# Optimization experiments

Hardware: AMD Instinct MI355X
Metric: run time of the kernel (lower is better)

## Reference

```python
import jax, jax.numpy as jnp
import numpy as np


def setup_inputs() -> dict:
    key = jax.random.key(0)
    kx, ke = jax.random.split(key)
    N, T, D, M = 64, 400, 1024, 256
    x = jax.random.normal(kx, (N, T, D), dtype=jnp.float32)
    embedding = jax.random.normal(ke, (M, D), dtype=jnp.float32)
    return {"x": x, "embedding": embedding}


def reference(x, embedding):
    # x: (N, T, D); embedding (codebook): (M, D)
    M, D = embedding.shape
    # L2_distance: normalize codebook rows, distances to detached x
    emb_norm = embedding / (jnp.linalg.norm(embedding, axis=1, keepdims=True) + 1e-4)
    x_flat = jax.lax.stop_gradient(x).reshape(-1, D)  # (N*T, D)
    distances = (jnp.sum(emb_norm ** 2, axis=1)[None, :]
                 + jnp.sum(x_flat ** 2, axis=1, keepdims=True)
                 - 2.0 * (x_flat @ emb_norm.T))  # (N*T, M)
    indices = jnp.argmin(distances, axis=-1)  # (N*T,)
    encodings = jax.nn.one_hot(indices, M, dtype=jnp.float32)  # (N*T, M)
    quantized = embedding[indices].reshape(x.shape)  # gather from UNnormalized codebook

    # commitment loss (both sides detached in original -> constant)
    commitment_loss = jnp.mean(
        (jax.lax.stop_gradient(x) - jax.lax.stop_gradient(quantized)) ** 2)

    # straight-through + average with quantized
    quantized_st = x + jax.lax.stop_gradient(quantized - x)
    quantized_ = (quantized_st + quantized) / 2.0

    avg_probs = jnp.mean(encodings, axis=0)  # (M,)
    perplexity = jnp.exp(-jnp.sum(avg_probs * jnp.log(avg_probs + 1e-10)))
    return quantized_, commitment_loss, perplexity
```

## Files before the change

### kernel.cpp

```cpp
#include <hip/hip_runtime.h>
#include <cstdint>
#include <cstddef>


typedef __attribute__((ext_vector_type(8))) short short8;
typedef __attribute__((ext_vector_type(4))) float f32x4;

namespace {
constexpr int kNT = 25600;
constexpr int kD  = 1024;
constexpr int kM  = 256;
constexpr size_t kQElems = (size_t)kNT * kD;

constexpr int WS_IMG_H = 0;
constexpr int WS_IMG_L = 131072;
constexpr int WS_E2N   = 262144;
constexpr int WS_SCL   = WS_E2N + kM;
constexpr int WS_E2R   = WS_SCL + kM;
constexpr int WS_COM   = WS_E2R + kM;
constexpr int WS_HIST  = WS_COM + 4;
constexpr int WS_ZERO_BYTES = (WS_HIST + kM - WS_COM) * 4;
}

typedef __attribute__((address_space(3))) unsigned int        lds_u32;
typedef const __attribute__((address_space(1))) unsigned int  glb_u32;

__device__ __forceinline__ void gl2lds16(const void* g, void* l) {
  __builtin_amdgcn_global_load_lds((glb_u32*)g, (lds_u32*)l, 16, 0, 0);
}

__global__ __launch_bounds__(256) void vq_normalize(const float* __restrict__ emb,
                                                    float* __restrict__ ws) {
  const int m = blockIdx.x;
  const int t = threadIdx.x;
  const float4 v = reinterpret_cast<const float4*>(emb + (size_t)m * kD)[t];
  float s = v.x * v.x + v.y * v.y + v.z * v.z + v.w * v.w;
#pragma unroll
  for (int mask = 32; mask >= 1; mask >>= 1) s += __shfl_xor(s, mask);
  __shared__ float red[4];
  if ((t & 63) == 0) red[t >> 6] = s;
  __syncthreads();
  const float tot = red[0] + red[1] + red[2] + red[3];
  const float sc  = sqrtf(tot) + 1e-4f;
  const float inv = 1.0f / sc;
  const float4 nv = make_float4(v.x * inv, v.y * inv, v.z * inv, v.w * inv);

  float s2 = nv.x * nv.x + nv.y * nv.y + nv.z * nv.z + nv.w * nv.w;
#pragma unroll
  for (int mask = 32; mask >= 1; mask >>= 1) s2 += __shfl_xor(s2, mask);
  __syncthreads();
  if ((t & 63) == 0) red[t >> 6] = s2;
  __syncthreads();
  if (t == 0) {
    ws[WS_E2N + m] = red[0] + red[1] + red[2] + red[3];
    ws[WS_SCL + m] = sc;
    ws[WS_E2R + m] = tot;
  }

  unsigned short* imgh = (unsigned short*)(ws + WS_IMG_H);
  unsigned short* imgl = (unsigned short*)(ws + WS_IMG_L);
  const int c  = t >> 3;
  const int g  = (t >> 1) & 3;
  const int sq = g ^ ((m >> 1) & 3);
  const int base = c * 8192 + m * 32 + sq * 8 + 4 * (t & 1);
  ushort4 hq, lq;
#pragma unroll
  for (int j = 0; j < 4; ++j) {
    const float fv = (&nv.x)[j];
    const unsigned int b = __float_as_uint(fv);
    const unsigned short hi = (unsigned short)(b >> 16);
    const float lof = fv - __uint_as_float(b & 0xFFFF0000u);
    const unsigned short lo = (unsigned short)(__float_as_uint(lof) >> 16);
    (&hq.x)[j] = hi; (&lq.x)[j] = lo;
  }
  *(ushort4*)(imgh + base) = hq;
  *(ushort4*)(imgl + base) = lq;
}

__global__ __launch_bounds__(256, 2) void vq_main(const float* __restrict__ x,
                                                  const float* __restrict__ emb,
                                                  const float* __restrict__ wsc,
                                                  float* __restrict__ out,
                                                  float* __restrict__ commit_sum,
                                                  int* __restrict__ hist) {
  __shared__ char pool[65536];
  __shared__ float e2n_s[kM], scl_s[kM], e2r_s[kM], x2s[64];
  __shared__ int idx_s[64];

  const int t  = threadIdx.x;
  const int l  = t & 63;
  const int w  = t >> 6;
  const int h  = w >> 1;
  const int rw = w & 1;
  const int r0 = blockIdx.x * 64;

  e2n_s[t] = wsc[WS_E2N + t];
  scl_s[t] = wsc[WS_SCL + t];
  e2r_s[t] = wsc[WS_E2R + t];

  const unsigned short* img = (const unsigned short*)(wsc + ((w & 1) ? WS_IMG_L : WS_IMG_H));
  char* myslot = pool + w * 16384;

  const int nlo = l & 15;
  const int sq  = (l >> 4) ^ ((l >> 1) & 3);
  const int rowA   = r0 + rw * 32 + nlo;
  const int kbase0 = h * 512 + ((l >> 4) << 3);

  f32x4 acc[2][16];
#pragma unroll
  for (int rt = 0; rt < 2; ++rt)
#pragma unroll
    for (int ct = 0; ct < 16; ++ct) acc[rt][ct] = (f32x4)0.0f;
  float x2[2] = {0.0f, 0.0f};

#pragma unroll 1
  for (int cc = 0; cc < 16; ++cc) {
    const unsigned short* src = img + (size_t)(h * 16 + cc) * 8192 + l * 8;
#pragma unroll
    for (int it = 0; it < 16; ++it)
      gl2lds16(src + it * 512, myslot + it * 1024);

    float4 f[2][2];
#pragma unroll
    for (int rt = 0; rt < 2; ++rt) {
      const float* xp = x + (size_t)(rowA + rt * 16) * kD + (cc * 32 + kbase0);
      f[rt][0] = *(const float4*)xp;
      f[rt][1] = *(const float4*)(xp + 4);
    }
    __syncthreads();

    short8 ah[2], al[2];
#pragma unroll
    for (int rt = 0; rt < 2; ++rt) {
      union { short8 v; unsigned short u[8]; } H, L;
#pragma unroll
      for (int j = 0; j < 8; ++j) {
        const float fv = (&f[rt][j >> 2].x)[j & 3];
        const unsigned int b = __float_as_uint(fv);
        H.u[j] = (unsigned short)(b >> 16);
        const float lof = fv - __uint_as_float(b & 0xFFFF0000u);
        L.u[j] = (unsigned short)(__float_as_uint(lof) >> 16);
        x2[rt] += fv * fv;
      }
      ah[rt] = H.v; al[rt] = L.v;
    }

    const char* bh_base = pool + (h * 2 + 0) * 16384;
    const char* bl_base = pool + (h * 2 + 1) * 16384;
#pragma unroll
    for (int ct = 0; ct < 16; ++ct) {
      const int off = (ct * 16 + nlo) * 64 + sq * 16;
      const short8 bh = *(const short8*)(bh_base + off);
      const short8 bl = *(const short8*)(bl_base + off);
#pragma unroll
      for (int rt = 0; rt < 2; ++rt) {
        acc[rt][ct] = __builtin_amdgcn_mfma_f32_16x16x32_bf16(ah[rt], bh, acc[rt][ct], 0, 0, 0);
        acc[rt][ct] = __builtin_amdgcn_mfma_f32_16x16x32_bf16(ah[rt], bl, acc[rt][ct], 0, 0, 0);
        acc[rt][ct] = __builtin_amdgcn_mfma_f32_16x16x32_bf16(al[rt], bh, acc[rt][ct], 0, 0, 0);
      }
    }
    __syncthreads();
  }

#pragma unroll
  for (int rt = 0; rt < 2; ++rt) {
    x2[rt] += __shfl_xor(x2[rt], 16);
    x2[rt] += __shfl_xor(x2[rt], 32);
  }

  float* Sd = (float*)pool;
  if (h == 0) {
#pragma unroll
    for (int rt = 0; rt < 2; ++rt) {
#pragma unroll
      for (int ct = 0; ct < 16; ++ct)
#pragma unroll
        for (int rg = 0; rg < 4; ++rg) {
          const int row = rw * 32 + rt * 16 + (l >> 4) * 4 + rg;
          Sd[row * 256 + ct * 16 + nlo] = -2.0f * acc[rt][ct][rg];
        }
      if (l < 16) x2s[rw * 32 + rt * 16 + l] = x2[rt];
    }
  }
  __syncthreads();
  if (h == 1) {
#pragma unroll
    for (int rt = 0; rt < 2; ++rt) {
#pragma unroll
      for (int ct = 0; ct < 16; ++ct)
#pragma unroll
        for (int rg = 0; rg < 4; ++rg) {
          const int row = rw * 32 + rt * 16 + (l >> 4) * 4 + rg;
          Sd[row * 256 + ct * 16 + nlo] -= 2.0f * acc[rt][ct][rg];
        }
      if (l < 16) x2s[rw * 32 + rt * 16 + l] += x2[rt];
    }
  }
  __syncthreads();

  {
    const int row = t >> 2, q = t & 3;
    float bv = 3.0e38f; int bj = 0;
    const float* Sr = Sd + row * 256 + q * 64;
    const float* En = e2n_s + q * 64;
    for (int jj = 0; jj < 64; ++jj) {
      const int jloc = (jj + 2 * row) & 63;
      const float v = En[jloc] + Sr[jloc];
      const int j = q * 64 + jloc;
      if (v < bv || (v == bv && j < bj)) { bv = v; bj = j; }
    }
#pragma unroll
    for (int m = 1; m <= 2; m <<= 1) {
      const float ov = __shfl_xor(bv, m);
      const int   oj = __shfl_xor(bj, m);
      if (ov < bv || (ov == bv && oj < bj)) { bv = ov; bj = oj; }
    }
    if (q == 0) {
      idx_s[row] = bj;
      atomicAdd(&hist[bj], 1);
      const float cl = x2s[row] + e2r_s[bj] - (e2n_s[bj] - bv) * scl_s[bj];
      atomicAdd(commit_sum, cl);
    }
  }
  __syncthreads();

  const float4* emb4 = reinterpret_cast<const float4*>(emb);
  float4* out4 = reinterpret_cast<float4*>(out);
#pragma unroll 4
  for (int i = 0; i < 64; ++i) {
    const int m = idx_s[i];
    out4[(size_t)(r0 + i) * (kD / 4) + t] = emb4[(size_t)m * (kD / 4) + t];
  }
}

__global__ __launch_bounds__(256) void vq_final(const int* __restrict__ hist,
                                                const float* __restrict__ commit_sum,
                                                float* __restrict__ out) {
  const int t = threadIdx.x;
  const float p = (float)hist[t] * (1.0f / (float)kNT);
  float s = p * logf(p + 1e-10f);
#pragma unroll
  for (int mask = 32; mask >= 1; mask >>= 1) s += __shfl_xor(s, mask);
  __shared__ float red[4];
  if ((t & 63) == 0) red[t >> 6] = s;
  __syncthreads();
  if (t == 0) {
    const float ent = red[0] + red[1] + red[2] + red[3];
    out[kQElems]     = commit_sum[0] * (1.0f / (float)kQElems);
    out[kQElems + 1] = expf(-ent);
  }
}

extern "C" void kernel_launch(void* const* d_in, const int* in_sizes, int n_in,
                              void* d_out, int out_size, void* d_ws, size_t ws_size,
                              hipStream_t stream) {
  (void)in_sizes; (void)n_in; (void)out_size; (void)ws_size;
  const float* x   = (const float*)d_in[0];
  const float* emb = (const float*)d_in[1];
  float* out = (float*)d_out;
  float* ws  = (float*)d_ws;

  hipMemsetAsync((char*)d_ws + (size_t)WS_COM * 4, 0, WS_ZERO_BYTES, stream);
  hipLaunchKernelGGL(vq_normalize, dim3(kM), dim3(256), 0, stream, emb, ws);
  hipLaunchKernelGGL(vq_main, dim3(kNT / 64), dim3(256), 0, stream,
                     x, emb, ws, out, ws + WS_COM, (int*)(ws + WS_HIST));
  hipLaunchKernelGGL(vq_final, dim3(1), dim3(256), 0, stream,
                     (const int*)(ws + WS_HIST), ws + WS_COM, out);
}
```

Baseline: 248.2 us.

## Double-buffer codebook tiles and give each wave full K range with register argmin

The main kernel is restructured so each wave owns 16 rows over the full K dimension instead of splitting K across wave pairs. This removes the LDS partial-sum reduction and the shared distance matrix; argmin is done in registers with cross-lane shuffles. Codebook tiles are double-buffered in LDS with async global-to-LDS loads, the next x chunk is prefetched, and hand-placed ds_read/waitcnt/sched_barrier interleave LDS reads with MFMAs. The gather/copy is done per wave. Risks include higher register pressure from 16 accumulators plus 16 prefetched B fragments, and fragile manual waitcnt counts.

```diff
diff --git a/kernel.cpp b/kernel.cpp
--- a/kernel.cpp
+++ b/kernel.cpp
@@ -24,9 +24,17 @@
 
 typedef __attribute__((address_space(3))) unsigned int        lds_u32;
 typedef const __attribute__((address_space(1))) unsigned int  glb_u32;
+typedef const __attribute__((address_space(3))) char          lds_chc;
 
 __device__ __forceinline__ void gl2lds16(const void* g, void* l) {
   __builtin_amdgcn_global_load_lds((glb_u32*)g, (lds_u32*)l, 16, 0, 0);
+}
+
+template <int OFF>
+__device__ __forceinline__ short8 ldsr(lds_chc* p) {
+  short8 r;
+  asm volatile("ds_read_b128 %0, %1 offset:%c2" : "=v"(r) : "v"(p), "i"(OFF));
+  return r;
 }
 
 __global__ __launch_bounds__(256) void vq_normalize(const float* __restrict__ emb,
@@ -77,159 +85,182 @@
   *(ushort4*)(imgl + base) = lq;
 }
 
+
+#define RD8(BSEL, G, H0, H1, H2, H3, L0, L1, L2, L3)                           \
+  H0 = ldsr<(BSEL) * 32768 + ((G) * 4 + 0) * 1024>(lbase);                     \
+  H1 = ldsr<(BSEL) * 32768 + ((G) * 4 + 1) * 1024>(lbase);                     \
+  H2 = ldsr<(BSEL) * 32768 + ((G) * 4 + 2) * 1024>(lbase);                     \
+  H3 = ldsr<(BSEL) * 32768 + ((G) * 4 + 3) * 1024>(lbase);                     \
+  L0 = ldsr<(BSEL) * 32768 + 16384 + ((G) * 4 + 0) * 1024>(lbase);             \
+  L1 = ldsr<(BSEL) * 32768 + 16384 + ((G) * 4 + 1) * 1024>(lbase);             \
+  L2 = ldsr<(BSEL) * 32768 + 16384 + ((G) * 4 + 2) * 1024>(lbase);             \
+  L3 = ldsr<(BSEL) * 32768 + 16384 + ((G) * 4 + 3) * 1024>(lbase);
+
+#define MM12(G, H0, H1, H2, H3, L0, L1, L2, L3)                                              \
+  acc[(G) * 4 + 0] = __builtin_amdgcn_mfma_f32_16x16x32_bf16(ah, H0, acc[(G) * 4 + 0], 0, 0, 0); \
+  acc[(G) * 4 + 1] = __builtin_amdgcn_mfma_f32_16x16x32_bf16(ah, H1, acc[(G) * 4 + 1], 0, 0, 0); \
+  acc[(G) * 4 + 2] = __builtin_amdgcn_mfma_f32_16x16x32_bf16(ah, H2, acc[(G) * 4 + 2], 0, 0, 0); \
+  acc[(G) * 4 + 3] = __builtin_amdgcn_mfma_f32_16x16x32_bf16(ah, H3, acc[(G) * 4 + 3], 0, 0, 0); \
+  acc[(G) * 4 + 0] = __builtin_amdgcn_mfma_f32_16x16x32_bf16(ah, L0, acc[(G) * 4 + 0], 0, 0, 0); \
+  acc[(G) * 4 + 1] = __builtin_amdgcn_mfma_f32_16x16x32_bf16(ah, L1, acc[(G) * 4 + 1], 0, 0, 0); \
+  acc[(G) * 4 + 2] = __builtin_amdgcn_mfma_f32_16x16x32_bf16(ah, L2, acc[(G) * 4 + 2], 0, 0, 0); \
+  acc[(G) * 4 + 3] = __builtin_amdgcn_mfma_f32_16x16x32_bf16(ah, L3, acc[(G) * 4 + 3], 0, 0, 0); \
+  acc[(G) * 4 + 0] = __builtin_amdgcn_mfma_f32_16x16x32_bf16(al, H0, acc[(G) * 4 + 0], 0, 0, 0); \
+  acc[(G) * 4 + 1] = __builtin_amdgcn_mfma_f32_16x16x32_bf16(al, H1, acc[(G) * 4 + 1], 0, 0, 0); \
+  acc[(G) * 4 + 2] = __builtin_amdgcn_mfma_f32_16x16x32_bf16(al, H2, acc[(G) * 4 + 2], 0, 0, 0); \
+  acc[(G) * 4 + 3] = __builtin_amdgcn_mfma_f32_16x16x32_bf16(al, H3, acc[(G) * 4 + 3], 0, 0, 0);
+
+#define VQ_ITER(KC, BSEL, XC0, XC1, XN0, XN1)                                  \
+  {                                                                            \
+    const int kcn_ = ((KC) < 31) ? (KC) + 1 : 31;                              \
+    const float* xp_ = xrow + kcn_ * 32;                                       \
+    XN0 = *(const float4*)xp_;                                                 \
+    XN1 = *(const float4*)(xp_ + 4);                                           \
+    {                                                                          \
+      const unsigned short* sg_ = simg + ((size_t)kcn_ << 13) + soff;          \
+      char* dg_ = &buf[(BSEL) ^ 1][0] + ldst;                                  \
+      _Pragma("unroll")                                                        \
+      for (int it_ = 0; it_ < 8; ++it_)                                        \
+        gl2lds16(sg_ + it_ * 512, dg_ + it_ * 1024);                           \
+    }                                                                          \
+    asm volatile("s_waitcnt vmcnt(10)" ::: "memory");                          \
+    __builtin_amdgcn_s_barrier();                                              \
+    asm volatile("" ::: "memory");                                             \
+    short8 ha0_, ha1_, ha2_, ha3_, la0_, la1_, la2_, la3_;                     \
+    short8 hb0_, hb1_, hb2_, hb3_, lb0_, lb1_, lb2_, lb3_;                     \
+    RD8((BSEL), 0, ha0_, ha1_, ha2_, ha3_, la0_, la1_, la2_, la3_)             \
+    RD8((BSEL), 1, hb0_, hb1_, hb2_, hb3_, lb0_, lb1_, lb2_, lb3_)             \
+    short8 ah, al;                                                             \
+    {                                                                          \
+      union { short8 v; unsigned short u[8]; } H_, L_;                         \
+      const float fx_[8] = {XC0.x, XC0.y, XC0.z, XC0.w,                        \
+                            XC1.x, XC1.y, XC1.z, XC1.w};                       \
+      _Pragma("unroll")                                                        \
+      for (int jj_ = 0; jj_ < 8; ++jj_) {                                      \
+        const float fv_ = fx_[jj_];                                            \
+        const unsigned int b_ = __float_as_uint(fv_);                          \
+        H_.u[jj_] = (unsigned short)(b_ >> 16);                                \
+        const float lo_ = fv_ - __uint_as_float(b_ & 0xFFFF0000u);             \
+        L_.u[jj_] = (unsigned short)(__float_as_uint(lo_) >> 16);              \
+        x2 += fv_ * fv_;                                                       \
+      }                                                                        \
+      ah = H_.v; al = L_.v;                                                    \
+    }                                                                          \
+    asm volatile("s_waitcnt lgkmcnt(8)" ::: "memory");                         \
+    __builtin_amdgcn_sched_barrier(0);                                         \
+    MM12(0, ha0_, ha1_, ha2_, ha3_, la0_, la1_, la2_, la3_)                    \
+    RD8((BSEL), 2, ha0_, ha1_, ha2_, ha3_, la0_, la1_, la2_, la3_)             \
+    asm volatile("s_waitcnt lgkmcnt(8)" ::: "memory");                         \
+    __builtin_amdgcn_sched_barrier(0);                                         \
+    MM12(1, hb0_, hb1_, hb2_, hb3_, lb0_, lb1_, lb2_, lb3_)                    \
+    RD8((BSEL), 3, hb0_, hb1_, hb2_, hb3_, lb0_, lb1_, lb2_, lb3_)             \
+    asm volatile("s_waitcnt lgkmcnt(8)" ::: "memory");                         \
+    __builtin_amdgcn_sched_barrier(0);                                         \
+    MM12(2, ha0_, ha1_, ha2_, ha3_, la0_, la1_, la2_, la3_)                    \
+    asm volatile("s_waitcnt lgkmcnt(0)" ::: "memory");                         \
+    __builtin_amdgcn_sched_barrier(0);                                         \
+    MM12(3, hb0_, hb1_, hb2_, hb3_, lb0_, lb1_, lb2_, lb3_)                    \
+    asm volatile("" ::: "memory");                                             \
+    __builtin_amdgcn_s_barrier();                                              \
+    asm volatile("" ::: "memory");                                             \
+  }
+
 __global__ __launch_bounds__(256, 2) void vq_main(const float* __restrict__ x,
                                                   const float* __restrict__ emb,
                                                   const float* __restrict__ wsc,
                                                   float* __restrict__ out,
                                                   float* __restrict__ commit_sum,
                                                   int* __restrict__ hist) {
-  __shared__ char pool[65536];
-  __shared__ float e2n_s[kM], scl_s[kM], e2r_s[kM], x2s[64];
-  __shared__ int idx_s[64];
-
-  const int t  = threadIdx.x;
-  const int l  = t & 63;
-  const int w  = t >> 6;
-  const int h  = w >> 1;
-  const int rw = w & 1;
-  const int r0 = blockIdx.x * 64;
-
-  e2n_s[t] = wsc[WS_E2N + t];
-  scl_s[t] = wsc[WS_SCL + t];
-  e2r_s[t] = wsc[WS_E2R + t];
-
-  const unsigned short* img = (const unsigned short*)(wsc + ((w & 1) ? WS_IMG_L : WS_IMG_H));
-  char* myslot = pool + w * 16384;
-
+  __shared__ char buf[2][32768];
+
+  const int t   = threadIdx.x;
+  const int l   = t & 63;
+  const int w   = t >> 6;
+  const int r0  = blockIdx.x * 64 + w * 16;
   const int nlo = l & 15;
-  const int sq  = (l >> 4) ^ ((l >> 1) & 3);
-  const int rowA   = r0 + rw * 32 + nlo;
-  const int kbase0 = h * 512 + ((l >> 4) << 3);
-
-  f32x4 acc[2][16];
-#pragma unroll
-  for (int rt = 0; rt < 2; ++rt)
-#pragma unroll
-    for (int ct = 0; ct < 16; ++ct) acc[rt][ct] = (f32x4)0.0f;
-  float x2[2] = {0.0f, 0.0f};
+  const int q   = l >> 4;
+  const int sq  = q ^ ((l >> 1) & 3);
+
+  const unsigned short* imgH = (const unsigned short*)(wsc + WS_IMG_H);
+  const unsigned short* imgL = (const unsigned short*)(wsc + WS_IMG_L);
+  const unsigned short* simg = (w & 2) ? imgL : imgH;
+  const int soff = (w & 1) * 4096 + l * 8;
+  const int ldst = w * 8192;
+
+  const float* xrow = x + (size_t)(r0 + nlo) * kD + q * 8;
+  lds_chc* lbase = (lds_chc*)&buf[0][0] + nlo * 64 + sq * 16;
+
+  f32x4 acc[16];
+#pragma unroll
+  for (int i = 0; i < 16; ++i) acc[i] = (f32x4)0.0f;
+  float x2 = 0.0f;
+
+  float4 xa0, xa1, xb0, xb1;
+  xa0 = *(const float4*)xrow;
+  xa1 = *(const float4*)(xrow + 4);
+  {
+    const unsigned short* sg = simg + soff;
+    char* dg = &buf[0][0] + ldst;
+#pragma unroll
+    for (int it = 0; it < 8; ++it) gl2lds16(sg + it * 512, dg + it * 1024);
+  }
 
 #pragma unroll 1
-  for (int cc = 0; cc < 16; ++cc) {
-    const unsigned short* src = img + (size_t)(h * 16 + cc) * 8192 + l * 8;
-#pragma unroll
-    for (int it = 0; it < 16; ++it)
-      gl2lds16(src + it * 512, myslot + it * 1024);
-
-    float4 f[2][2];
-#pragma unroll
-    for (int rt = 0; rt < 2; ++rt) {
-      const float* xp = x + (size_t)(rowA + rt * 16) * kD + (cc * 32 + kbase0);
-      f[rt][0] = *(const float4*)xp;
-      f[rt][1] = *(const float4*)(xp + 4);
+  for (int kk = 0; kk < 32; kk += 2) {
+    VQ_ITER(kk,     0, xa0, xa1, xb0, xb1)
+    VQ_ITER(kk + 1, 1, xb0, xb1, xa0, xa1)
+  }
+
+  x2 += __shfl_xor(x2, 16);
+  x2 += __shfl_xor(x2, 32);
+
+  float bv[4] = {3.0e38f, 3.0e38f, 3.0e38f, 3.0e38f};
+  int   bj[4] = {0, 0, 0, 0};
+#pragma unroll
+  for (int ct = 0; ct < 16; ++ct) {
+    const int j = ct * 16 + nlo;
+    const float e = wsc[WS_E2N + j];
+#pragma unroll
+    for (int rg = 0; rg < 4; ++rg) {
+      const float v = e - 2.0f * acc[ct][rg];
+      if (v < bv[rg] || (v == bv[rg] && j < bj[rg])) { bv[rg] = v; bj[rg] = j; }
     }
-    __syncthreads();
-
-    short8 ah[2], al[2];
-#pragma unroll
-    for (int rt = 0; rt < 2; ++rt) {
-      union { short8 v; unsigned short u[8]; } H, L;
-#pragma unroll
-      for (int j = 0; j < 8; ++j) {
-        const float fv = (&f[rt][j >> 2].x)[j & 3];
-        const unsigned int b = __float_as_uint(fv);
-        H.u[j] = (unsigned short)(b >> 16);
-        const float lof = fv - __uint_as_float(b & 0xFFFF0000u);
-        L.u[j] = (unsigned short)(__float_as_uint(lof) >> 16);
-        x2[rt] += fv * fv;
-      }
-      ah[rt] = H.v; al[rt] = L.v;
+  }
+#pragma unroll
+  for (int mk = 1; mk <= 8; mk <<= 1) {
+#pragma unroll
+    for (int rg = 0; rg < 4; ++rg) {
+      const float ov = __shfl_xor(bv[rg], mk);
+      const int   oj = __shfl_xor(bj[rg], mk);
+      if (ov < bv[rg] || (ov == bv[rg] && oj < bj[rg])) { bv[rg] = ov; bj[rg] = oj; }
     }
-
-    const char* bh_base = pool + (h * 2 + 0) * 16384;
-    const char* bl_base = pool + (h * 2 + 1) * 16384;
-#pragma unroll
-    for (int ct = 0; ct < 16; ++ct) {
-      const int off = (ct * 16 + nlo) * 64 + sq * 16;
-      const short8 bh = *(const short8*)(bh_base + off);
-      const short8 bl = *(const short8*)(bl_base + off);
-#pragma unroll
-      for (int rt = 0; rt < 2; ++rt) {
-        acc[rt][ct] = __builtin_amdgcn_mfma_f32_16x16x32_bf16(ah[rt], bh, acc[rt][ct], 0, 0, 0);
-        acc[rt][ct] = __builtin_amdgcn_mfma_f32_16x16x32_bf16(ah[rt], bl, acc[rt][ct], 0, 0, 0);
-        acc[rt][ct] = __builtin_amdgcn_mfma_f32_16x16x32_bf16(al[rt], bh, acc[rt][ct], 0, 0, 0);
-      }
-    }
-    __syncthreads();
-  }
-
-#pragma unroll
-  for (int rt = 0; rt < 2; ++rt) {
-    x2[rt] += __shfl_xor(x2[rt], 16);
-    x2[rt] += __shfl_xor(x2[rt], 32);
-  }
-
-  float* Sd = (float*)pool;
-  if (h == 0) {
-#pragma unroll
-    for (int rt = 0; rt < 2; ++rt) {
-#pragma unroll
-      for (int ct = 0; ct < 16; ++ct)
-#pragma unroll
-        for (int rg = 0; rg < 4; ++rg) {
-          const int row = rw * 32 + rt * 16 + (l >> 4) * 4 + rg;
-          Sd[row * 256 + ct * 16 + nlo] = -2.0f * acc[rt][ct][rg];
-        }
-      if (l < 16) x2s[rw * 32 + rt * 16 + l] = x2[rt];
-    }
-  }
-  __syncthreads();
-  if (h == 1) {
-#pragma unroll
-    for (int rt = 0; rt < 2; ++rt) {
-#pragma unroll
-      for (int ct = 0; ct < 16; ++ct)
-#pragma unroll
-        for (int rg = 0; rg < 4; ++rg) {
-          const int row = rw * 32 + rt * 16 + (l >> 4) * 4 + rg;
-          Sd[row * 256 + ct * 16 + nlo] -= 2.0f * acc[rt][ct][rg];
-        }
-      if (l < 16) x2s[rw * 32 + rt * 16 + l] += x2[rt];
-    }
-  }
-  __syncthreads();
-
-  {
-    const int row = t >> 2, q = t & 3;
-    float bv = 3.0e38f; int bj = 0;
-    const float* Sr = Sd + row * 256 + q * 64;
-    const float* En = e2n_s + q * 64;
-    for (int jj = 0; jj < 64; ++jj) {
-      const int jloc = (jj + 2 * row) & 63;
-      const float v = En[jloc] + Sr[jloc];
-      const int j = q * 64 + jloc;
-      if (v < bv || (v == bv && j < bj)) { bv = v; bj = j; }
-    }
-#pragma unroll
-    for (int m = 1; m <= 2; m <<= 1) {
-      const float ov = __shfl_xor(bv, m);
-      const int   oj = __shfl_xor(bj, m);
-      if (ov < bv || (ov == bv && oj < bj)) { bv = ov; bj = oj; }
-    }
-    if (q == 0) {
-      idx_s[row] = bj;
-      atomicAdd(&hist[bj], 1);
-      const float cl = x2s[row] + e2r_s[bj] - (e2n_s[bj] - bv) * scl_s[bj];
-      atomicAdd(commit_sum, cl);
-    }
-  }
-  __syncthreads();
-
-  const float4* emb4 = reinterpret_cast<const float4*>(emb);
-  float4* out4 = reinterpret_cast<float4*>(out);
-#pragma unroll 4
-  for (int i = 0; i < 64; ++i) {
-    const int m = idx_s[i];
-    out4[(size_t)(r0 + i) * (kD / 4) + t] = emb4[(size_t)m * (kD / 4) + t];
+  }
+
+  float clq = 0.0f;
+#pragma unroll
+  for (int rg = 0; rg < 4; ++rg) {
+    const int j = bj[rg];
+    const float xr2 = __shfl(x2, (q << 2) | rg);
+    clq += xr2 + wsc[WS_E2R + j] - (wsc[WS_E2N + j] - bv[rg]) * wsc[WS_SCL + j];
+  }
+  if (nlo == 0) {
+#pragma unroll
+    for (int rg = 0; rg < 4; ++rg) atomicAdd(&hist[bj[rg]], 1);
+  }
+  float cs = (nlo == 0) ? clq : 0.0f;
+  cs += __shfl_xor(cs, 16);
+  cs += __shfl_xor(cs, 32);
+  if (l == 0) atomicAdd(commit_sum, cs);
+
+  const float4* emb4 = (const float4*)emb;
+  float4* out4 = (float4*)out;
+#pragma unroll
+  for (int r = 0; r < 16; ++r) {
+    const int j = __shfl(bj[r & 3], (r >> 2) << 4);
+    const float4* s = emb4 + (size_t)j * (kD / 4);
+    float4* d = out4 + (size_t)(r0 + r) * (kD / 4);
+#pragma unroll
+    for (int c = 0; c < 4; ++c) d[c * 64 + l] = s[c * 64 + l];
   }
 }
 
```

Measured after the change: 252.6 us. No clear change (+1.8%).
